# Optimization experiments

Measured on AMD Instinct MI355X. Metric: run time of the kernel, lower is better.

## Reference

```python
import jax, jax.numpy as jnp
import numpy as np

E = 8        # num_experts
K = 2        # top_k routing
D = 1024     # d_model
F = 4096     # expert hidden (ffn) dim
EPS = 1e-5


def _layernorm(h, g, b):
    # h: [E, T, C]; g, b: [E, C]
    mu = h.mean(axis=-1, keepdims=True)
    var = ((h - mu) ** 2).mean(axis=-1, keepdims=True)
    return (h - mu) * jax.lax.rsqrt(var + EPS) * g[:, None, :] + b[:, None, :]


def setup_inputs() -> dict:
    key = jax.random.key(0)
    ks = jax.random.split(key, 8)
    B, S = 2, 2048
    x = jax.random.normal(ks[0], (B, S, D), dtype=jnp.float32)
    Wr = jax.random.normal(ks[1], (D, E), dtype=jnp.float32) / np.sqrt(D)
    br = jnp.zeros((E,), dtype=jnp.float32)
    W1 = jax.random.normal(ks[2], (E, D, F), dtype=jnp.float32) / np.sqrt(D)
    b1 = jnp.zeros((E, F), dtype=jnp.float32)
    g1 = jnp.ones((E, F), dtype=jnp.float32)
    be1 = jnp.zeros((E, F), dtype=jnp.float32)
    W2 = jax.random.normal(ks[3], (E, F, D), dtype=jnp.float32) / np.sqrt(F)
    b2 = jnp.zeros((E, D), dtype=jnp.float32)
    g2 = jnp.ones((E, D), dtype=jnp.float32)
    be2 = jnp.zeros((E, D), dtype=jnp.float32)
    return {"x": x, "Wr": Wr, "br": br, "W1": W1, "b1": b1, "g1": g1,
            "be1": be1, "W2": W2, "b2": b2, "g2": g2, "be2": be2}


def reference(x, Wr, br, W1, b1, g1, be1, W2, b2, g2, be2):
    B, S, _ = x.shape
    xt = x.reshape(-1, D)                       # [T, D] token matrix
    # --- router + sampler: top-k softmax probs, renormalized over the k slots
    logits = xt @ Wr + br                       # [T, E]
    p = jax.nn.softmax(logits, axis=-1)
    probs, idx = jax.lax.top_k(p, K)            # [T, K]
    probs = probs / probs.sum(axis=-1, keepdims=True)
    # --- experts layer 1: Linear -> relu -> LayerNorm, per expert
    h = jnp.einsum('td,edf->etf', xt, W1) + b1[:, None, :]   # [E, T, F]
    h = _layernorm(jax.nn.relu(h), g1, be1)
    # --- experts layer 2: Linear -> relu -> LayerNorm
    y = jnp.einsum('etf,efd->etd', h, W2) + b2[:, None, :]   # [E, T, D]
    y = _layernorm(jax.nn.relu(y), g2, be2)
    # --- weighted scatter-combine: gate[t,e] = sum_k 1[idx[t,k]==e] * probs[t,k]
    gate = (jax.nn.one_hot(idx, E, dtype=x.dtype) * probs[..., None]).sum(axis=1)  # [T, E]
    out = jnp.einsum('te,etd->td', gate, y)     # index_add combine, dense form
    return out.reshape(B, S, D)
```

## Files before the change

### kernel.cpp

```cpp
#include <hip/hip_runtime.h>


#define E_N 8
#define TOPK 2
#define DM 1024
#define FF 4096
#define NTOK 4096
#define NA 8192
#define LN_EPS 1e-5f
#define NBX 128

typedef __attribute__((ext_vector_type(4))) float f32x4;
typedef __attribute__((ext_vector_type(8))) short short8;

__device__ __forceinline__ unsigned short f2bf(float f) {
    unsigned int u = __builtin_bit_cast(unsigned int, f);
    u = (u + 0x7FFFu + ((u >> 16) & 1u)) >> 16;
    return (unsigned short)u;
}
__device__ __forceinline__ float bf2f(unsigned short h) {
    unsigned int u = ((unsigned int)h) << 16;
    return __builtin_bit_cast(float, u);
}
__device__ __forceinline__ void unp(unsigned int u, float& lo, float& hi) {
    lo = bf2f((unsigned short)(u & 0xffffu));
    hi = bf2f((unsigned short)(u >> 16));
}
__device__ __forceinline__ unsigned int pk(float lo, float hi) {
    return (unsigned int)f2bf(lo) | ((unsigned int)f2bf(hi) << 16);
}

__device__ __forceinline__ void gload16(const unsigned short* g, unsigned short* lds) {
    __builtin_amdgcn_global_load_lds(
        (const __attribute__((address_space(1))) unsigned int*)g,
        (__attribute__((address_space(3))) unsigned int*)lds, 16, 0, 0);
}


__global__ __launch_bounds__(256) void k_prep(
        const float* __restrict__ W1, const float* __restrict__ W2,
        unsigned short* __restrict__ W1T, unsigned short* __restrict__ W2T,
        const float* __restrict__ x, const float* __restrict__ Wr,
        const float* __restrict__ br, unsigned short* __restrict__ xb,
        int* __restrict__ topk_idx, float* __restrict__ topk_p)
{
    __shared__ float tile[64][65];
    int z = blockIdx.z;
    int tid = threadIdx.x;

    if (z == 16) {
        int wv = tid >> 6, lane = tid & 63;
        int t = blockIdx.x * 4 + wv;
        const float* xr = x + (size_t)t * DM;
        unsigned short* xbr = xb + (size_t)t * DM;
        float a0=0,a1=0,a2=0,a3=0,a4=0,a5=0,a6=0,a7=0;
        for (int d = lane; d < DM; d += 64) {
            float xv = xr[d];
            xbr[d] = f2bf(xv);
            const float4* wp = (const float4*)(Wr + d * 8);
            float4 w0 = wp[0], w1 = wp[1];
            a0 += xv * w0.x; a1 += xv * w0.y; a2 += xv * w0.z; a3 += xv * w0.w;
            a4 += xv * w1.x; a5 += xv * w1.y; a6 += xv * w1.z; a7 += xv * w1.w;
        }
#pragma unroll
        for (int off = 32; off; off >>= 1) {
            a0 += __shfl_xor(a0, off); a1 += __shfl_xor(a1, off);
            a2 += __shfl_xor(a2, off); a3 += __shfl_xor(a3, off);
            a4 += __shfl_xor(a4, off); a5 += __shfl_xor(a5, off);
            a6 += __shfl_xor(a6, off); a7 += __shfl_xor(a7, off);
        }
        if (lane == 0) {
            float l[8] = {a0 + br[0], a1 + br[1], a2 + br[2], a3 + br[3],
                          a4 + br[4], a5 + br[5], a6 + br[6], a7 + br[7]};
            int i0 = 0;
#pragma unroll
            for (int e = 1; e < 8; e++) if (l[e] > l[i0]) i0 = e;
            int i1 = (i0 == 0) ? 1 : 0;
#pragma unroll
            for (int e = 0; e < 8; e++) if (e != i0 && l[e] > l[i1]) i1 = e;
            float p1 = expf(l[i1] - l[i0]);
            float s = 1.0f + p1;
            topk_idx[2 * t]     = i0;
            topk_idx[2 * t + 1] = i1;
            topk_p[2 * t]       = 1.0f / s;
            topk_p[2 * t + 1]   = p1 / s;
        }
        return;
    }

    const float* src; unsigned short* dst; int R, C, bx, by;
    if (z < 8) {
        R = DM; C = FF;
        src = W1 + (size_t)z * R * C;  dst = W1T + (size_t)z * R * C;
        bx = blockIdx.x & 63; by = blockIdx.x >> 6;
    } else {
        R = FF; C = DM;
        src = W2 + (size_t)(z - 8) * R * C;  dst = W2T + (size_t)(z - 8) * R * C;
        bx = blockIdx.x & 15; by = blockIdx.x >> 4;
    }
    const float* s = src + (size_t)(by * 64) * C + bx * 64;
    unsigned short* d = dst + (size_t)(bx * 64) * R + by * 64;
    int lr = tid >> 4, lc = (tid & 15) * 4;
#pragma unroll
    for (int p = 0; p < 4; p++) {
        float4 v = *(const float4*)(s + (size_t)(lr + p * 16) * C + lc);
        tile[lr + p * 16][lc] = v.x;     tile[lr + p * 16][lc + 1] = v.y;
        tile[lr + p * 16][lc + 2] = v.z; tile[lr + p * 16][lc + 3] = v.w;
    }
    __syncthreads();
    int rc = (tid & 7) * 8;
#pragma unroll
    for (int p = 0; p < 2; p++) {
        int cc = (tid >> 3) + p * 32;
        float a0 = tile[rc + 0][cc], a1 = tile[rc + 1][cc];
        float a2 = tile[rc + 2][cc], a3 = tile[rc + 3][cc];
        float a4 = tile[rc + 4][cc], a5 = tile[rc + 5][cc];
        float a6 = tile[rc + 6][cc], a7 = tile[rc + 7][cc];
        uint4 o;
        o.x = pk(a0, a1); o.y = pk(a2, a3); o.z = pk(a4, a5); o.w = pk(a6, a7);
        *(uint4*)(d + (size_t)cc * R + rc) = o;
    }
}


__global__ __launch_bounds__(256) void k_route2(const int* __restrict__ topk_idx,
        int* __restrict__ cnt, int* __restrict__ offs,
        int* __restrict__ assign_tok, int* __restrict__ assign_e,
        int* __restrict__ slot)
{
    __shared__ int h[8], base[8];
    int tid = threadIdx.x;
    if (tid < 8) h[tid] = 0;
    __syncthreads();
    int el[32];
#pragma unroll
    for (int i = 0; i < 32; i++) {
        int idx = tid * 32 + i;
        el[i] = topk_idx[idx];
        atomicAdd(&h[el[i]], 1);
    }
    __syncthreads();
    if (tid == 0) {
        int s = 0;
        for (int e = 0; e < E_N; e++) { offs[e] = s; cnt[e] = h[e]; base[e] = s; s += h[e]; }
        offs[E_N] = s;
    }
    __syncthreads();
    if (tid < 8) h[tid] = base[tid];
    __syncthreads();
#pragma unroll
    for (int i = 0; i < 32; i++) {
        int idx = tid * 32 + i;
        int e = el[i];
        int pos = atomicAdd(&h[e], 1);
        assign_tok[pos] = idx >> 1;
        assign_e[pos] = e;
        slot[idx] = pos;
    }
}


template<bool GATHER, bool EPI>
__global__ __launch_bounds__(256, 4) void k_gemm(
    const unsigned short* __restrict__ A,
    const unsigned short* __restrict__ BT,
    const float* __restrict__ bias,
    unsigned short* __restrict__ C,
    const int* __restrict__ cnt, const int* __restrict__ offs,
    const int* __restrict__ gather_tok,
    int Kslice, int N, int ldA, int ldB, int GX, int KS, size_t slicePitch)
{
    __shared__ __align__(1024) char lds[32768];

    int bid = blockIdx.x;
    int e = bid & 7;
    int lb = bid >> 3;
    int M = cnt[e];
    if (M <= 0) return;
    int off_e = offs[e];
    int nrows = (M + 127) >> 7;
    int ntiles = nrows * GX * KS;

    int tid = threadIdx.x;
    int wv = tid >> 6, lane = tid & 63;
    int lr = lane & 15, hi = lane >> 4;
    int mW = (wv >> 1) * 64, nW = (wv & 1) * 64;
    int colsw = ((lane & 7) ^ (lane >> 3)) * 8;
    int l3 = lane >> 3;
    int nt = Kslice >> 6;

    for (int t = lb; t < ntiles; t += NBX) {
        int r = t % nrows;
        int q = t / nrows;
        int xn = q % GX;
        int ks = q / GX;
        int m0 = r * 128;
        int n0 = xn * 128;
        int kbase = ks * Kslice;

        const unsigned short* aptr[4];
        const unsigned short* bptr[4];
#pragma unroll
        for (int i = 0; i < 4; i++) {
            int j = wv * 4 + i;
            int rr = m0 + j * 8 + l3; rr = (rr < M) ? rr : (M - 1);
            size_t arow = GATHER ? (size_t)gather_tok[off_e + rr] : (size_t)(off_e + rr);
            aptr[i] = A + arow * (size_t)ldA + kbase + colsw;
            int rb = n0 + j * 8 + l3;
            bptr[i] = BT + ((size_t)e * N + rb) * (size_t)ldB + kbase + colsw;
        }

        f32x4 acc[4][4];
        f32x4 zz = {0.f, 0.f, 0.f, 0.f};
#pragma unroll
        for (int mi = 0; mi < 4; mi++)
#pragma unroll
            for (int ni = 0; ni < 4; ni++) acc[mi][ni] = zz;

        for (int kt = 0; kt < nt; ++kt) {
            __syncthreads();
#pragma unroll
            for (int i = 0; i < 4; i++) {
                gload16(aptr[i] + kt * 64, (unsigned short*)(lds + (wv * 4 + i) * 1024));
                gload16(bptr[i] + kt * 64, (unsigned short*)(lds + 16384 + (wv * 4 + i) * 1024));
            }
            __syncthreads();
#pragma unroll
            for (int kss = 0; kss < 2; kss++) {
                int cb = (kss * 64 + hi * 16) ^ ((lr & 7) << 4);
                short8 afr[4], bfr[4];
#pragma unroll
                for (int ni = 0; ni < 4; ni++)
                    bfr[ni] = *(const short8*)(lds + 16384 + (nW + ni * 16 + lr) * 128 + cb);
#pragma unroll
                for (int mi = 0; mi < 4; mi++)
                    afr[mi] = *(const short8*)(lds + (mW + mi * 16 + lr) * 128 + cb);
                __builtin_amdgcn_s_setprio(1);
#pragma unroll
                for (int mi = 0; mi < 4; mi++)
#pragma unroll
                    for (int ni = 0; ni < 4; ni++)
                        acc[mi][ni] = __builtin_amdgcn_mfma_f32_16x16x32_bf16(
                            afr[mi], bfr[ni], acc[mi][ni], 0, 0, 0);
                __builtin_amdgcn_s_setprio(0);
            }
        }

        unsigned short* Cs = C + ks * slicePitch;
        float bv[4] = {0.f, 0.f, 0.f, 0.f};
        if (EPI) {
#pragma unroll
            for (int ni = 0; ni < 4; ni++)
                bv[ni] = bias[(size_t)e * N + (n0 + nW + ni * 16 + lr)];
        }
#pragma unroll
        for (int mi = 0; mi < 4; mi++) {
            int mb = m0 + mW + mi * 16 + hi * 4;
#pragma unroll
            for (int rr = 0; rr < 4; rr++) {
                int m = mb + rr;
                if (m < M) {
                    unsigned short* crow = Cs + (size_t)(off_e + m) * N;
#pragma unroll
                    for (int ni = 0; ni < 4; ni++) {
                        float v = acc[mi][ni][rr];
                        if (EPI) v = fmaxf(v + bv[ni], 0.0f);
                        crow[n0 + nW + ni * 16 + lr] = f2bf(v);
                    }
                }
            }
        }
    }
}


__global__ __launch_bounds__(256) void k_ln1(unsigned short* __restrict__ H,
        const float* __restrict__ g, const float* __restrict__ b,
        const int* __restrict__ assign_e)
{
    size_t a = blockIdx.x;
    int e = assign_e[a];
    unsigned short* row = H + a * FF;
    int tid = threadIdx.x;
    uint4 u0 = *(const uint4*)(row + tid * 16);
    uint4 u1 = *(const uint4*)(row + tid * 16 + 8);
    float v[16];
    unp(u0.x, v[0], v[1]);  unp(u0.y, v[2], v[3]);
    unp(u0.z, v[4], v[5]);  unp(u0.w, v[6], v[7]);
    unp(u1.x, v[8], v[9]);  unp(u1.y, v[10], v[11]);
    unp(u1.z, v[12], v[13]); unp(u1.w, v[14], v[15]);
    float s = 0.f, q = 0.f;
#pragma unroll
    for (int i = 0; i < 16; i++) { s += v[i]; q += v[i] * v[i]; }
#pragma unroll
    for (int off = 32; off; off >>= 1) { s += __shfl_xor(s, off); q += __shfl_xor(q, off); }
    __shared__ float red[8];
    int wv = tid >> 6, lane = tid & 63;
    if (lane == 0) { red[wv * 2] = s; red[wv * 2 + 1] = q; }
    __syncthreads();
    s = red[0] + red[2] + red[4] + red[6];
    q = red[1] + red[3] + red[5] + red[7];
    float mu = s * (1.0f / FF);
    float var = q * (1.0f / FF) - mu * mu;
    float rstd = rsqrtf(var + LN_EPS);
    const float* gg = g + (size_t)e * FF + tid * 16;
    const float* bb = b + (size_t)e * FF + tid * 16;
    float4 G0 = *(const float4*)(gg);      float4 G1 = *(const float4*)(gg + 4);
    float4 G2 = *(const float4*)(gg + 8);  float4 G3 = *(const float4*)(gg + 12);
    float4 B0 = *(const float4*)(bb);      float4 B1 = *(const float4*)(bb + 4);
    float4 B2 = *(const float4*)(bb + 8);  float4 B3 = *(const float4*)(bb + 12);
    float gvv[16] = {G0.x,G0.y,G0.z,G0.w,G1.x,G1.y,G1.z,G1.w,G2.x,G2.y,G2.z,G2.w,G3.x,G3.y,G3.z,G3.w};
    float bvv[16] = {B0.x,B0.y,B0.z,B0.w,B1.x,B1.y,B1.z,B1.w,B2.x,B2.y,B2.z,B2.w,B3.x,B3.y,B3.z,B3.w};
#pragma unroll
    for (int i = 0; i < 16; i++) v[i] = (v[i] - mu) * rstd * gvv[i] + bvv[i];
    u0.x = pk(v[0], v[1]);  u0.y = pk(v[2], v[3]);
    u0.z = pk(v[4], v[5]);  u0.w = pk(v[6], v[7]);
    u1.x = pk(v[8], v[9]);  u1.y = pk(v[10], v[11]);
    u1.z = pk(v[12], v[13]); u1.w = pk(v[14], v[15]);
    *(uint4*)(row + tid * 16) = u0;
    *(uint4*)(row + tid * 16 + 8) = u1;
}


__global__ __launch_bounds__(256) void k_comb(const unsigned short* __restrict__ Yp,
        const float* __restrict__ g, const float* __restrict__ b2,
        const float* __restrict__ be,
        const int* __restrict__ slot, const float* __restrict__ topk_p,
        const int* __restrict__ assign_e, float* __restrict__ out)
{
    int t = blockIdx.x;
    int s0 = slot[2 * t], s1 = slot[2 * t + 1];
    float p0 = topk_p[2 * t], p1 = topk_p[2 * t + 1];
    int e0 = assign_e[s0], e1 = assign_e[s1];
    int tid = threadIdx.x;
    int d = tid * 4;
    const unsigned short* Y1 = Yp + (size_t)NA * DM;
    uint2 ua0 = *(const uint2*)(Yp + (size_t)s0 * DM + d);
    uint2 ua1 = *(const uint2*)(Y1 + (size_t)s0 * DM + d);
    uint2 ub0 = *(const uint2*)(Yp + (size_t)s1 * DM + d);
    uint2 ub1 = *(const uint2*)(Y1 + (size_t)s1 * DM + d);
    float4 bza = *(const float4*)(b2 + (size_t)e0 * DM + d);
    float4 bzb = *(const float4*)(b2 + (size_t)e1 * DM + d);
    float x0, x1, y0, y1;
    float va[4], vb[4];
    unp(ua0.x, x0, x1); unp(ua1.x, y0, y1);
    va[0] = fmaxf(x0 + y0 + bza.x, 0.f); va[1] = fmaxf(x1 + y1 + bza.y, 0.f);
    unp(ua0.y, x0, x1); unp(ua1.y, y0, y1);
    va[2] = fmaxf(x0 + y0 + bza.z, 0.f); va[3] = fmaxf(x1 + y1 + bza.w, 0.f);
    unp(ub0.x, x0, x1); unp(ub1.x, y0, y1);
    vb[0] = fmaxf(x0 + y0 + bzb.x, 0.f); vb[1] = fmaxf(x1 + y1 + bzb.y, 0.f);
    unp(ub0.y, x0, x1); unp(ub1.y, y0, y1);
    vb[2] = fmaxf(x0 + y0 + bzb.z, 0.f); vb[3] = fmaxf(x1 + y1 + bzb.w, 0.f);

    float sa = 0.f, qa = 0.f, sb = 0.f, qb = 0.f;
#pragma unroll
    for (int i = 0; i < 4; i++) {
        sa += va[i]; qa += va[i] * va[i];
        sb += vb[i]; qb += vb[i] * vb[i];
    }
#pragma unroll
    for (int off = 32; off; off >>= 1) {
        sa += __shfl_xor(sa, off); qa += __shfl_xor(qa, off);
        sb += __shfl_xor(sb, off); qb += __shfl_xor(qb, off);
    }
    __shared__ float red[16];
    int wv = tid >> 6, lane = tid & 63;
    if (lane == 0) { red[wv*4+0]=sa; red[wv*4+1]=qa; red[wv*4+2]=sb; red[wv*4+3]=qb; }
    __syncthreads();
    sa = red[0] + red[4] + red[8]  + red[12];
    qa = red[1] + red[5] + red[9]  + red[13];
    sb = red[2] + red[6] + red[10] + red[14];
    qb = red[3] + red[7] + red[11] + red[15];
    float mua = sa * (1.0f / DM), vara = qa * (1.0f / DM) - mua * mua;
    float ra = rsqrtf(vara + LN_EPS);
    float mub = sb * (1.0f / DM), varb = qb * (1.0f / DM) - mub * mub;
    float rb = rsqrtf(varb + LN_EPS);
    float4 ga  = *(const float4*)(g + (size_t)e0 * DM + d);
    float4 ba  = *(const float4*)(be + (size_t)e0 * DM + d);
    float4 gb4 = *(const float4*)(g + (size_t)e1 * DM + d);
    float4 bb4 = *(const float4*)(be + (size_t)e1 * DM + d);
    float4 o;
    o.x = p0 * ((va[0] - mua) * ra * ga.x + ba.x) + p1 * ((vb[0] - mub) * rb * gb4.x + bb4.x);
    o.y = p0 * ((va[1] - mua) * ra * ga.y + ba.y) + p1 * ((vb[1] - mub) * rb * gb4.y + bb4.y);
    o.z = p0 * ((va[2] - mua) * ra * ga.z + ba.z) + p1 * ((vb[2] - mub) * rb * gb4.z + bb4.z);
    o.w = p0 * ((va[3] - mua) * ra * ga.w + ba.w) + p1 * ((vb[3] - mub) * rb * gb4.w + bb4.w);
    *(float4*)(out + (size_t)t * DM + d) = o;
}


extern "C" void kernel_launch(void* const* d_in, const int* in_sizes, int n_in,
                              void* d_out, int out_size, void* d_ws, size_t ws_size,
                              hipStream_t stream) {
    const float* x   = (const float*)d_in[0];
    const float* Wr  = (const float*)d_in[1];
    const float* br  = (const float*)d_in[2];
    const float* W1  = (const float*)d_in[3];
    const float* b1  = (const float*)d_in[4];
    const float* g1  = (const float*)d_in[5];
    const float* be1 = (const float*)d_in[6];
    const float* W2  = (const float*)d_in[7];
    const float* b2  = (const float*)d_in[8];
    const float* g2  = (const float*)d_in[9];
    const float* be2 = (const float*)d_in[10];
    float* out = (float*)d_out;

    char* w = (char*)d_ws;
    int*   cnt        = (int*)(w);
    int*   offs       = (int*)(w + 128);
    int*   topk_idx   = (int*)(w + 512);
    float* topk_p     = (float*)(w + 512 + (32 << 10));
    int*   assign_tok = (int*)(w + 512 + (64 << 10));
    int*   assign_e   = (int*)(w + 512 + (96 << 10));
    int*   slot       = (int*)(w + 512 + (128 << 10));
    unsigned short* xb  = (unsigned short*)(w + ((size_t)1 << 20));
    unsigned short* W1T = (unsigned short*)(w + ((size_t)9 << 20));
    unsigned short* W2T = (unsigned short*)(w + ((size_t)73 << 20));
    unsigned short* Hb  = (unsigned short*)(w + ((size_t)137 << 20));
    unsigned short* Yp  = (unsigned short*)(w + ((size_t)201 << 20));

    k_prep<<<dim3(1024, 1, 17), 256, 0, stream>>>(
        W1, W2, W1T, W2T, x, Wr, br, xb, topk_idx, topk_p);
    k_route2<<<1, 256, 0, stream>>>(topk_idx, cnt, offs, assign_tok, assign_e, slot);
    k_gemm<true, true><<<8 * NBX, 256, 0, stream>>>(
        xb, W1T, b1, Hb, cnt, offs, assign_tok, DM, FF, DM, DM, 32, 1, 0);
    k_ln1<<<NA, 256, 0, stream>>>(Hb, g1, be1, assign_e);
    k_gemm<false, false><<<8 * NBX, 256, 0, stream>>>(
        Hb, W2T, nullptr, Yp, cnt, offs, nullptr, FF / 2, DM, FF, FF, 8, 2,
        (size_t)NA * DM);
    k_comb<<<NTOK, 256, 0, stream>>>(Yp, g2, b2, be2, slot, topk_p, assign_e, out);
}
```

Before: 333.1 us.

## Overlap W2 transpose with first expert GEMM and swizzle transpose tiles

Moves the fp32-to-bf16 transpose of W2 out of the prep kernel and into the tail of the first grouped GEMM's persistent tile loop, so the weight conversion runs alongside GEMM1 instead of before it. The transpose is factored into a helper that uses an XOR-swizzled unpadded LDS tile with float4 stores and float2 reads. The router/x-cast path is also vectorised with float4 loads. This adds extra work and an LDS reuse barrier inside the GEMM blocks, and the transpose only runs for experts with nonzero token counts.

Result: no change. 335.1 us (+0.6%).

```diff
diff --git a/kernel.cpp b/kernel.cpp
--- a/kernel.cpp
+++ b/kernel.cpp
@@ -36,31 +36,66 @@
         (__attribute__((address_space(3))) unsigned int*)lds, 16, 0, 0);
 }
 
+__device__ __forceinline__ void transpose64(const float* __restrict__ s, int sld,
+                                            unsigned short* __restrict__ d, int dld,
+                                            float* tile) {
+    int tid = threadIdx.x;
+    int lr = tid >> 4, lc = (tid & 15) * 4;
+#pragma unroll
+    for (int p = 0; p < 4; p++) {
+        int r = lr + p * 16;
+        float4 v = *(const float4*)(s + (size_t)r * sld + lc);
+        *(float4*)&tile[r * 64 + (lc ^ (((r >> 3) & 7) << 2))] = v;
+    }
+    __syncthreads();
+    int a = tid & 7;
+    int col = (tid >> 3) * 2;
+    int cbase = (col & ~3) ^ (a << 2);
+    int clo = col & 3;
+    unsigned int o0[4], o1[4];
+#pragma unroll
+    for (int i = 0; i < 8; i += 2) {
+        int r0 = 8 * a + i;
+        float2 xy0 = *(const float2*)&tile[r0 * 64 + cbase + clo];
+        float2 xy1 = *(const float2*)&tile[(r0 + 1) * 64 + cbase + clo];
+        o0[i >> 1] = pk(xy0.x, xy1.x);
+        o1[i >> 1] = pk(xy0.y, xy1.y);
+    }
+    *(uint4*)(d + (size_t)col * dld + 8 * a) = *(uint4*)o0;
+    *(uint4*)(d + (size_t)(col + 1) * dld + 8 * a) = *(uint4*)o1;
+}
+
 
 __global__ __launch_bounds__(256) void k_prep(
-        const float* __restrict__ W1, const float* __restrict__ W2,
-        unsigned short* __restrict__ W1T, unsigned short* __restrict__ W2T,
+        const float* __restrict__ W1, unsigned short* __restrict__ W1T,
         const float* __restrict__ x, const float* __restrict__ Wr,
         const float* __restrict__ br, unsigned short* __restrict__ xb,
         int* __restrict__ topk_idx, float* __restrict__ topk_p)
 {
-    __shared__ float tile[64][65];
+    __shared__ float tile[64 * 64];
     int z = blockIdx.z;
     int tid = threadIdx.x;
 
-    if (z == 16) {
+    if (z == 8) {
         int wv = tid >> 6, lane = tid & 63;
         int t = blockIdx.x * 4 + wv;
         const float* xr = x + (size_t)t * DM;
         unsigned short* xbr = xb + (size_t)t * DM;
         float a0=0,a1=0,a2=0,a3=0,a4=0,a5=0,a6=0,a7=0;
-        for (int d = lane; d < DM; d += 64) {
-            float xv = xr[d];
-            xbr[d] = f2bf(xv);
-            const float4* wp = (const float4*)(Wr + d * 8);
-            float4 w0 = wp[0], w1 = wp[1];
-            a0 += xv * w0.x; a1 += xv * w0.y; a2 += xv * w0.z; a3 += xv * w0.w;
-            a4 += xv * w1.x; a5 += xv * w1.y; a6 += xv * w1.z; a7 += xv * w1.w;
+#pragma unroll
+        for (int p = 0; p < 4; p++) {
+            int d0 = p * 256 + lane * 4;
+            float4 xv = *(const float4*)(xr + d0);
+            uint2 pkd; pkd.x = pk(xv.x, xv.y); pkd.y = pk(xv.z, xv.w);
+            *(uint2*)(xbr + d0) = pkd;
+            float xs[4] = {xv.x, xv.y, xv.z, xv.w};
+#pragma unroll
+            for (int j = 0; j < 4; j++) {
+                const float4* wp = (const float4*)(Wr + (d0 + j) * 8);
+                float4 w0 = wp[0], w1 = wp[1];
+                a0 += xs[j] * w0.x; a1 += xs[j] * w0.y; a2 += xs[j] * w0.z; a3 += xs[j] * w0.w;
+                a4 += xs[j] * w1.x; a5 += xs[j] * w1.y; a6 += xs[j] * w1.z; a7 += xs[j] * w1.w;
+            }
         }
 #pragma unroll
         for (int off = 32; off; off >>= 1) {
@@ -88,38 +123,10 @@
         return;
     }
 
-    const float* src; unsigned short* dst; int R, C, bx, by;
-    if (z < 8) {
-        R = DM; C = FF;
-        src = W1 + (size_t)z * R * C;  dst = W1T + (size_t)z * R * C;
-        bx = blockIdx.x & 63; by = blockIdx.x >> 6;
-    } else {
-        R = FF; C = DM;
-        src = W2 + (size_t)(z - 8) * R * C;  dst = W2T + (size_t)(z - 8) * R * C;
-        bx = blockIdx.x & 15; by = blockIdx.x >> 4;
-    }
-    const float* s = src + (size_t)(by * 64) * C + bx * 64;
-    unsigned short* d = dst + (size_t)(bx * 64) * R + by * 64;
-    int lr = tid >> 4, lc = (tid & 15) * 4;
-#pragma unroll
-    for (int p = 0; p < 4; p++) {
-        float4 v = *(const float4*)(s + (size_t)(lr + p * 16) * C + lc);
-        tile[lr + p * 16][lc] = v.x;     tile[lr + p * 16][lc + 1] = v.y;
-        tile[lr + p * 16][lc + 2] = v.z; tile[lr + p * 16][lc + 3] = v.w;
-    }
-    __syncthreads();
-    int rc = (tid & 7) * 8;
-#pragma unroll
-    for (int p = 0; p < 2; p++) {
-        int cc = (tid >> 3) + p * 32;
-        float a0 = tile[rc + 0][cc], a1 = tile[rc + 1][cc];
-        float a2 = tile[rc + 2][cc], a3 = tile[rc + 3][cc];
-        float a4 = tile[rc + 4][cc], a5 = tile[rc + 5][cc];
-        float a6 = tile[rc + 6][cc], a7 = tile[rc + 7][cc];
-        uint4 o;
-        o.x = pk(a0, a1); o.y = pk(a2, a3); o.z = pk(a4, a5); o.w = pk(a6, a7);
-        *(uint4*)(d + (size_t)cc * R + rc) = o;
-    }
+    int bx = blockIdx.x & 63, by = blockIdx.x >> 6;
+    transpose64(W1 + (size_t)z * DM * FF + (size_t)(by * 64) * FF + bx * 64, FF,
+                W1T + (size_t)z * DM * FF + (size_t)(bx * 64) * DM + by * 64, DM,
+                tile);
 }
 
 
@@ -160,7 +167,7 @@
 }
 
 
-template<bool GATHER, bool EPI>
+template<bool GATHER, bool EPI, bool TRANS>
 __global__ __launch_bounds__(256, 4) void k_gemm(
     const unsigned short* __restrict__ A,
     const unsigned short* __restrict__ BT,
@@ -168,6 +175,7 @@
     unsigned short* __restrict__ C,
     const int* __restrict__ cnt, const int* __restrict__ offs,
     const int* __restrict__ gather_tok,
+    const float* __restrict__ Wsrc, unsigned short* __restrict__ Wdst,
     int Kslice, int N, int ldA, int ldB, int GX, int KS, size_t slicePitch)
 {
     __shared__ __align__(1024) char lds[32768];
@@ -179,7 +187,8 @@
     if (M <= 0) return;
     int off_e = offs[e];
     int nrows = (M + 127) >> 7;
-    int ntiles = nrows * GX * KS;
+    int ntiles_g = nrows * GX * KS;
+    int ntiles = ntiles_g + (TRANS ? 1024 : 0);
 
     int tid = threadIdx.x;
     int wv = tid >> 6, lane = tid & 63;
@@ -190,6 +199,16 @@
     int nt = Kslice >> 6;
 
     for (int t = lb; t < ntiles; t += NBX) {
+        if (TRANS && t >= ntiles_g) {
+            int tt = t - ntiles_g;
+            int bx = tt & 15, by = tt >> 4;
+            __syncthreads();
+            transpose64(Wsrc + (size_t)e * FF * DM + (size_t)(by * 64) * DM + bx * 64, DM,
+                        Wdst + (size_t)e * DM * FF + (size_t)(bx * 64) * FF + by * 64, FF,
+                        (float*)lds);
+            continue;
+        }
+
         int r = t % nrows;
         int q = t / nrows;
         int xn = q % GX;
@@ -418,14 +437,15 @@
     unsigned short* Hb  = (unsigned short*)(w + ((size_t)137 << 20));
     unsigned short* Yp  = (unsigned short*)(w + ((size_t)201 << 20));
 
-    k_prep<<<dim3(1024, 1, 17), 256, 0, stream>>>(
-        W1, W2, W1T, W2T, x, Wr, br, xb, topk_idx, topk_p);
+    k_prep<<<dim3(1024, 1, 9), 256, 0, stream>>>(
+        W1, W1T, x, Wr, br, xb, topk_idx, topk_p);
     k_route2<<<1, 256, 0, stream>>>(topk_idx, cnt, offs, assign_tok, assign_e, slot);
-    k_gemm<true, true><<<8 * NBX, 256, 0, stream>>>(
-        xb, W1T, b1, Hb, cnt, offs, assign_tok, DM, FF, DM, DM, 32, 1, 0);
+    k_gemm<true, true, true><<<8 * NBX, 256, 0, stream>>>(
+        xb, W1T, b1, Hb, cnt, offs, assign_tok, W2, W2T,
+        DM, FF, DM, DM, 32, 1, 0);
     k_ln1<<<NA, 256, 0, stream>>>(Hb, g1, be1, assign_e);
-    k_gemm<false, false><<<8 * NBX, 256, 0, stream>>>(
-        Hb, W2T, nullptr, Yp, cnt, offs, nullptr, FF / 2, DM, FF, FF, 8, 2,
-        (size_t)NA * DM);
+    k_gemm<false, false, false><<<8 * NBX, 256, 0, stream>>>(
+        Hb, W2T, nullptr, Yp, cnt, offs, nullptr, nullptr, nullptr,
+        FF / 2, DM, FF, FF, 8, 2, (size_t)NA * DM);
     k_comb<<<NTOK, 256, 0, stream>>>(Yp, g2, b2, be2, slot, topk_p, assign_e, out);
 }
```
